# Performance work log

Hardware: AMD Instinct MI355X
Metric: run time of the kernel (lower is better)

Reference implementation:

```python
import jax, jax.numpy as jnp
import numpy as np

B, T, D, H = 128, 512, 1024, 1024


def setup_inputs() -> dict:
    key = jax.random.key(0)
    k_x, k_wx, k_wh = jax.random.split(key, 3)
    # PyTorch Linear init scale ~ U(-1/sqrt(fan_in), 1/sqrt(fan_in)); normal*0.03 is fine for a numeric baseline
    x = jax.random.normal(k_x, (B, T, D), dtype=jnp.float32)
    adjacency = jnp.zeros((T, T), dtype=jnp.float32)  # accepted by the torch module but unused
    Wx = jax.random.normal(k_wx, (4, D, H), dtype=jnp.float32) * (1.0 / np.sqrt(D))
    Wh = jax.random.normal(k_wh, (4, H, H), dtype=jnp.float32) * (1.0 / np.sqrt(H))
    b = jnp.zeros((4, H), dtype=jnp.float32)
    return {"x": x, "adjacency": adjacency, "Wx": Wx, "Wh": Wh, "b": b}


def _tree_lstm(x, Wx, Wh, b):
    # x: [B, T, D]; gate order: i, f, o, u
    xt = jnp.transpose(x, (1, 0, 2))  # [T, B, D]
    # precompute all input projections in one big batched GEMM: [T, 4, B, H]
    x_gates = jnp.einsum('tbd,gdh->tgbh', xt, Wx)
    h0 = jnp.zeros((x.shape[0], Wh.shape[1]), dtype=x.dtype)
    c0 = jnp.zeros_like(h0)

    def step(carry, xg_t):
        h, c = carry
        gates = xg_t + jnp.einsum('bh,ghk->gbk', h, Wh) + b[:, None, :]  # [4, B, H]
        i_t = jax.nn.sigmoid(gates[0])
        f_t = jax.nn.sigmoid(gates[1])
        o_t = jax.nn.sigmoid(gates[2])
        u_t = jnp.tanh(gates[3])
        c_new = f_t * c + i_t * u_t
        h_new = o_t * jnp.tanh(c_new)  # dropout is identity at inference
        return (h_new, c_new), None

    (h, _), _ = jax.lax.scan(step, (h0, c0), x_gates)
    return h  # [B, H]


def reference(x, adjacency, Wx, Wh, b):
    del adjacency  # unused in the original forward
    return _tree_lstm(x, Wx, Wh, b)
```

## Files before the change

kernel.cpp:

```cpp
#include <hip/hip_runtime.h>
#include <hip/hip_bf16.h>

typedef __attribute__((ext_vector_type(8))) short bf16x8;
typedef __attribute__((ext_vector_type(4))) float f32x4;
typedef __attribute__((ext_vector_type(2))) unsigned uint32x2;

#define NBLK 256
#define NTHR 512

__device__ __forceinline__ unsigned short f2bf(float f) {
  unsigned int u = __float_as_uint(f);
  unsigned int r = (u + 0x7FFFu + ((u >> 16) & 1u)) >> 16;
  return (unsigned short)r;
}

__device__ __forceinline__ bf16x8 ldg_b128_coh(const unsigned short* p) {
  bf16x8 r;
  asm volatile("global_load_dwordx4 %0, %1, off sc0 sc1"
               : "=v"(r) : "v"(p) : "memory");
  return r;
}
__device__ __forceinline__ void stg_b16_coh(unsigned short* p, unsigned v) {
  asm volatile("global_store_short %0, %1, off sc0 sc1"
               :: "v"(p), "v"(v) : "memory");
}

__global__ __launch_bounds__(256) void pack_w(const float* __restrict__ Wx,
                                              const float* __restrict__ Wh,
                                              unsigned short* __restrict__ Wp) {
  int idx = blockIdx.x * 256 + threadIdx.x;
  int k  = idx & 2047;
  int c  = (idx >> 11) & 31;
  int jb = idx >> 16;
  int g  = c & 3;
  int j  = jb * 8 + (c >> 2);
  float v = (k < 1024) ? Wh[((size_t)(g * 1024 + k)) * 1024 + j]
                       : Wx[((size_t)(g * 1024 + (k - 1024))) * 1024 + j];
  Wp[idx] = f2bf(v);
}

__global__ __launch_bounds__(256) void pack_x(const float* __restrict__ x,
                                              unsigned short* __restrict__ xpk) {
  size_t idx = (size_t)blockIdx.x * 256 + threadIdx.x;
  int lane = (int)(idx & 63);
  int wr   = (int)((idx >> 6) & 3);
  int s    = (int)((idx >> 8) & 15);
  int wn   = (int)((idx >> 12) & 1);
  int rb   = (int)((idx >> 13) & 1);
  int t    = (int)(idx >> 14);
  int a15 = lane & 15, hi = lane >> 4;
  int row = rb * 64 + wr * 16 + a15;
  int k   = (2 * s + wn) * 32 + hi * 8;
  const float* src = x + ((size_t)row * 512 + t) * 1024 + k;
  float4 f0 = *(const float4*)src;
  float4 f1 = *(const float4*)(src + 4);
  float fl[8] = {f0.x, f0.y, f0.z, f0.w, f1.x, f1.y, f1.z, f1.w};
  union { bf16x8 v; unsigned short us[8]; } u;
  #pragma unroll
  for (int e = 0; e < 8; ++e) u.us[e] = f2bf(fl[e]);
  *(bf16x8*)(xpk + idx * 8) = u.v;
}

__global__ __launch_bounds__(512, 2) void lstm_persist(
    const float* __restrict__ x,
    const unsigned short* __restrict__ xpk,
    const unsigned short* __restrict__ Wp,
    const float* __restrict__ bias,
    unsigned short* __restrict__ h0,
    unsigned short* __restrict__ h1,
    float* __restrict__ out,
    unsigned* __restrict__ bar)
{
  __shared__ unsigned short Wlds[32][2052];
  __shared__ float gt[2][64][33];

  const int tid = threadIdx.x;
  const int bx  = blockIdx.x;
  const int xcd = bx & 7;
  const int rb  = xcd >> 2;
  const int jb  = (bx >> 3) * 4 + (xcd & 3);
  const int row0 = rb * 64;

  #pragma unroll
  for (int rep = 0; rep < 16; ++rep) {
    int ch = rep * 512 + tid;
    int c  = ch >> 8;
    int k8 = (ch & 255) * 8;
    *(bf16x8*)&Wlds[c][k8] = *(const bf16x8*)(Wp + ((size_t)(jb * 32 + c)) * 2048 + k8);
  }

  const int lane = tid & 63;
  const int w    = tid >> 6;
  const int wr   = w >> 1;
  const int wn   = w & 1;
  const int a15  = lane & 15;
  const int hi   = lane >> 4;

  const int um  = tid >> 3;
  const int uj  = tid & 7;
  const int ujg = jb * 8 + uj;
  const float bi = bias[ujg], bf_ = bias[1024 + ujg];
  const float bo = bias[2048 + ujg], bu = bias[3072 + ujg];
  float creg = 0.f;

  const int rowg = row0 + wr * 16 + a15;
  const float* xrow = x + (size_t)rowg * 512 * 1024;
  const size_t xpk_lane = ((size_t)wr * 64 + lane) * 8;
  const unsigned* fpoll = bar + rb * 128 + (lane << 1);

  __syncthreads();

  unsigned short* hb[2] = {h0, h1};
  bf16x8 xreg[16];

  if (xpk) {
    const unsigned short* xs = xpk + (((size_t)0 * 2 + rb) * 2 + wn) * 16 * 2048 + xpk_lane;
    #pragma unroll
    for (int s = 0; s < 16; ++s)
      asm volatile("global_load_dwordx4 %0, %1, off" : "=v"(xreg[s]) : "v"(xs + s * 2048) : "memory");
    asm volatile("s_waitcnt vmcnt(0)" ::: "memory");
    __builtin_amdgcn_sched_barrier(0);
  } else {
    const float* xt = xrow + hi * 8;
    #pragma unroll
    for (int s = 0; s < 16; ++s) {
      const float* xp = xt + (2 * s + wn) * 32;
      float4 f0 = *(const float4*)xp;
      float4 f1 = *(const float4*)(xp + 4);
      float fl[8] = {f0.x, f0.y, f0.z, f0.w, f1.x, f1.y, f1.z, f1.w};
      union { bf16x8 v; unsigned short us[8]; } u;
      #pragma unroll
      for (int e = 0; e < 8; ++e) u.us[e] = f2bf(fl[e]);
      xreg[s] = u.v;
    }
  }

  for (int t = 0; t < 512; ++t) {
    const unsigned short* hc = hb[t & 1];
    unsigned short* hn = hb[(t + 1) & 1];

    bf16x8 hreg[16];
    const unsigned short* hbase = hc + (size_t)rowg * 1024 + hi * 8;
    #pragma unroll
    for (int s = 0; s < 16; ++s)
      hreg[s] = ldg_b128_coh(hbase + (2 * s + wn) * 32);
    __builtin_amdgcn_sched_barrier(0);

    f32x4 acc0 = {}, acc1 = {};
    #pragma unroll
    for (int s = 0; s < 16; ++s) {
      const int kk = 1024 + (2 * s + wn) * 32 + hi * 8;
      bf16x8 b0 = *(const bf16x8*)&Wlds[a15][kk];
      bf16x8 b1 = *(const bf16x8*)&Wlds[16 + a15][kk];
      acc0 = __builtin_amdgcn_mfma_f32_16x16x32_bf16(xreg[s], b0, acc0, 0, 0, 0);
      acc1 = __builtin_amdgcn_mfma_f32_16x16x32_bf16(xreg[s], b1, acc1, 0, 0, 0);
    }

    asm volatile("s_waitcnt vmcnt(8)" ::: "memory");
    __builtin_amdgcn_sched_barrier(0);
    #pragma unroll
    for (int s = 0; s < 8; ++s) {
      const int kk = (2 * s + wn) * 32 + hi * 8;
      bf16x8 b0 = *(const bf16x8*)&Wlds[a15][kk];
      bf16x8 b1 = *(const bf16x8*)&Wlds[16 + a15][kk];
      acc0 = __builtin_amdgcn_mfma_f32_16x16x32_bf16(hreg[s], b0, acc0, 0, 0, 0);
      acc1 = __builtin_amdgcn_mfma_f32_16x16x32_bf16(hreg[s], b1, acc1, 0, 0, 0);
    }
    asm volatile("s_waitcnt vmcnt(0)" ::: "memory");
    __builtin_amdgcn_sched_barrier(0);
    #pragma unroll
    for (int s = 8; s < 16; ++s) {
      const int kk = (2 * s + wn) * 32 + hi * 8;
      bf16x8 b0 = *(const bf16x8*)&Wlds[a15][kk];
      bf16x8 b1 = *(const bf16x8*)&Wlds[16 + a15][kk];
      acc0 = __builtin_amdgcn_mfma_f32_16x16x32_bf16(hreg[s], b0, acc0, 0, 0, 0);
      acc1 = __builtin_amdgcn_mfma_f32_16x16x32_bf16(hreg[s], b1, acc1, 0, 0, 0);
    }

    #pragma unroll
    for (int r = 0; r < 4; ++r) {
      gt[wn][wr * 16 + hi * 4 + r][a15]      = acc0[r];
      gt[wn][wr * 16 + hi * 4 + r][16 + a15] = acc1[r];
    }
    __syncthreads();

    float vi = gt[0][um][uj * 4 + 0] + gt[1][um][uj * 4 + 0] + bi;
    float vf = gt[0][um][uj * 4 + 1] + gt[1][um][uj * 4 + 1] + bf_;
    float vo = gt[0][um][uj * 4 + 2] + gt[1][um][uj * 4 + 2] + bo;
    float vu = gt[0][um][uj * 4 + 3] + gt[1][um][uj * 4 + 3] + bu;
    float iv = 1.f / (1.f + expf(-vi));
    float fv = 1.f / (1.f + expf(-vf));
    float ov = 1.f / (1.f + expf(-vo));
    float uv = tanhf(vu);
    creg = fv * creg + iv * uv;
    float hv = ov * tanhf(creg);
    stg_b16_coh(hn + (size_t)(row0 + um) * 1024 + ujg, (unsigned)f2bf(hv));
    if (t == 511) {
      out[(size_t)(row0 + um) * 1024 + ujg] = hv;
      break;
    }

    asm volatile("s_waitcnt vmcnt(0)" ::: "memory");
    __builtin_amdgcn_s_barrier();
    if (tid == 0) {
      const unsigned* p = bar + rb * 128 + jb;
      unsigned val = (unsigned)(t + 1);
      asm volatile("global_store_dword %0, %1, off sc0 sc1"
                   :: "v"(p), "v"(val) : "memory");
    }

    if (xpk) {
      const unsigned short* xs = xpk + (((size_t)(t + 1) * 2 + rb) * 2 + wn) * 16 * 2048 + xpk_lane;
      #pragma unroll
      for (int s = 0; s < 16; ++s)
        asm volatile("global_load_dwordx4 %0, %1, off" : "=v"(xreg[s]) : "v"(xs + s * 2048) : "memory");
    } else {
      const float* xt = xrow + (size_t)(t + 1) * 1024 + hi * 8;
      #pragma unroll
      for (int s = 0; s < 16; ++s) {
        const float* xp = xt + (2 * s + wn) * 32;
        float4 f0 = *(const float4*)xp;
        float4 f1 = *(const float4*)(xp + 4);
        float fl[8] = {f0.x, f0.y, f0.z, f0.w, f1.x, f1.y, f1.z, f1.w};
        union { bf16x8 v; unsigned short us[8]; } u;
        #pragma unroll
        for (int e = 0; e < 8; ++e) u.us[e] = f2bf(fl[e]);
        xreg[s] = u.v;
      }
    }

    for (;;) {
      uint32x2 v;
      asm volatile("global_load_dwordx2 %0, %1, off sc0 sc1"
                   : "=v"(v) : "v"(fpoll) : "memory");
      asm volatile("s_waitcnt vmcnt(0)" ::: "memory");
      if (__all(v.x > (unsigned)t && v.y > (unsigned)t)) break;
      __builtin_amdgcn_s_sleep(1);
    }
    __builtin_amdgcn_sched_barrier(0);
  }
}

extern "C" void kernel_launch(void* const* d_in, const int* in_sizes, int n_in,
                              void* d_out, int out_size, void* d_ws, size_t ws_size,
                              hipStream_t stream) {
  const float* x    = (const float*)d_in[0];
  const float* Wx   = (const float*)d_in[2];
  const float* Wh   = (const float*)d_in[3];
  const float* bias = (const float*)d_in[4];
  float* out = (float*)d_out;

  char* ws = (char*)d_ws;
  unsigned short* Wp = (unsigned short*)ws;
  unsigned short* h0 = (unsigned short*)(ws + 16777216);
  unsigned short* h1 = h0 + 128 * 1024;
  unsigned* bar = (unsigned*)(ws + 16777216 + 2 * 262144);
  const size_t XPK_OFF = 33554432;
  const size_t XPK_SZ  = 134217728;
  unsigned short* xpk = (ws_size >= XPK_OFF + XPK_SZ)
                        ? (unsigned short*)(ws + XPK_OFF) : nullptr;

  pack_w<<<32768, 256, 0, stream>>>(Wx, Wh, Wp);
  if (xpk) pack_x<<<32768, 256, 0, stream>>>(x, xpk);
  hipMemsetAsync(h0, 0, 128 * 1024 * sizeof(unsigned short), stream);
  hipMemsetAsync(bar, 0, 4096, stream);

  (void)in_sizes; (void)n_in;
  lstm_persist<<<NBLK, NTHR, 0, stream>>>(x, xpk, Wp, bias, h0, h1, out, bar);
}
```

Baseline: 3.797 ms.

## Use per-warp fine-grained flags and overlap x-projection with recurrent wait

Replaces the single per-block step flag with per-warp flags, so consumers poll flags for each K-chunk of h and issue loads for chunks as soon as their producers finish, instead of waiting for all blocks. The x-projection MFMAs for the next step are computed right after the gate update and prefetched two steps ahead, moving them off the critical path between barriers. Step 0 skips the h GEMM, so the h0 memset is dropped. This raises flag-polling traffic and control-flow complexity in exchange for less time waiting on the global barrier.

```diff
diff --git a/kernel.cpp b/kernel.cpp
--- a/kernel.cpp
+++ b/kernel.cpp
@@ -106,75 +106,101 @@
   const int rowg = row0 + wr * 16 + a15;
   const float* xrow = x + (size_t)rowg * 512 * 1024;
   const size_t xpk_lane = ((size_t)wr * 64 + lane) * 8;
-  const unsigned* fpoll = bar + rb * 128 + (lane << 1);
+
+  const unsigned* fp0 = bar + (rb * 8 + 2 * wr    ) * 128 + 2 * lane;
+  const unsigned* fp1 = bar + (rb * 8 + 2 * wr + 1) * 128 + 2 * lane;
+  unsigned* fprod = bar + (rb * 8 + w) * 128 + jb;
 
   __syncthreads();
 
   unsigned short* hb[2] = {h0, h1};
   bf16x8 xreg[16];
-
-  if (xpk) {
-    const unsigned short* xs = xpk + (((size_t)0 * 2 + rb) * 2 + wn) * 16 * 2048 + xpk_lane;
-    #pragma unroll
-    for (int s = 0; s < 16; ++s)
-      asm volatile("global_load_dwordx4 %0, %1, off" : "=v"(xreg[s]) : "v"(xs + s * 2048) : "memory");
-    asm volatile("s_waitcnt vmcnt(0)" ::: "memory");
-    __builtin_amdgcn_sched_barrier(0);
-  } else {
-    const float* xt = xrow + hi * 8;
-    #pragma unroll
-    for (int s = 0; s < 16; ++s) {
-      const float* xp = xt + (2 * s + wn) * 32;
-      float4 f0 = *(const float4*)xp;
-      float4 f1 = *(const float4*)(xp + 4);
-      float fl[8] = {f0.x, f0.y, f0.z, f0.w, f1.x, f1.y, f1.z, f1.w};
-      union { bf16x8 v; unsigned short us[8]; } u;
+  f32x4 acc0 = {}, acc1 = {};
+
+  auto xload = [&](int tt) {
+    if (xpk) {
+      const unsigned short* xs = xpk + ((((size_t)tt * 2 + rb) * 2 + wn) * 16) * 2048 + xpk_lane;
       #pragma unroll
-      for (int e = 0; e < 8; ++e) u.us[e] = f2bf(fl[e]);
-      xreg[s] = u.v;
-    }
+      for (int s = 0; s < 16; ++s)
+        asm volatile("global_load_dwordx4 %0, %1, off"
+                     : "=v"(xreg[s]) : "v"(xs + s * 2048) : "memory");
+    } else {
+      const float* xt = xrow + (size_t)tt * 1024 + hi * 8;
+      #pragma unroll
+      for (int s = 0; s < 16; ++s) {
+        const float* xp = xt + (2 * s + wn) * 32;
+        float4 f0 = *(const float4*)xp;
+        float4 f1 = *(const float4*)(xp + 4);
+        float fl[8] = {f0.x, f0.y, f0.z, f0.w, f1.x, f1.y, f1.z, f1.w};
+        union { bf16x8 v; unsigned short us[8]; } u;
+        #pragma unroll
+        for (int e = 0; e < 8; ++e) u.us[e] = f2bf(fl[e]);
+        xreg[s] = u.v;
+      }
+    }
+  };
+
+  xload(0);
+  asm volatile("s_waitcnt vmcnt(0)" ::: "memory");
+  __builtin_amdgcn_sched_barrier(0);
+  #pragma unroll
+  for (int s = 0; s < 16; ++s) {
+    const int kk = 1024 + (2 * s + wn) * 32 + hi * 8;
+    bf16x8 b0 = *(const bf16x8*)&Wlds[a15][kk];
+    bf16x8 b1 = *(const bf16x8*)&Wlds[16 + a15][kk];
+    acc0 = __builtin_amdgcn_mfma_f32_16x16x32_bf16(xreg[s], b0, acc0, 0, 0, 0);
+    acc1 = __builtin_amdgcn_mfma_f32_16x16x32_bf16(xreg[s], b1, acc1, 0, 0, 0);
   }
+  xload(1);
 
   for (int t = 0; t < 512; ++t) {
     const unsigned short* hc = hb[t & 1];
     unsigned short* hn = hb[(t + 1) & 1];
 
-    bf16x8 hreg[16];
-    const unsigned short* hbase = hc + (size_t)rowg * 1024 + hi * 8;
-    #pragma unroll
-    for (int s = 0; s < 16; ++s)
-      hreg[s] = ldg_b128_coh(hbase + (2 * s + wn) * 32);
-    __builtin_amdgcn_sched_barrier(0);
-
-    f32x4 acc0 = {}, acc1 = {};
-    #pragma unroll
-    for (int s = 0; s < 16; ++s) {
-      const int kk = 1024 + (2 * s + wn) * 32 + hi * 8;
-      bf16x8 b0 = *(const bf16x8*)&Wlds[a15][kk];
-      bf16x8 b1 = *(const bf16x8*)&Wlds[16 + a15][kk];
-      acc0 = __builtin_amdgcn_mfma_f32_16x16x32_bf16(xreg[s], b0, acc0, 0, 0, 0);
-      acc1 = __builtin_amdgcn_mfma_f32_16x16x32_bf16(xreg[s], b1, acc1, 0, 0, 0);
-    }
-
-    asm volatile("s_waitcnt vmcnt(8)" ::: "memory");
-    __builtin_amdgcn_sched_barrier(0);
-    #pragma unroll
-    for (int s = 0; s < 8; ++s) {
-      const int kk = (2 * s + wn) * 32 + hi * 8;
-      bf16x8 b0 = *(const bf16x8*)&Wlds[a15][kk];
-      bf16x8 b1 = *(const bf16x8*)&Wlds[16 + a15][kk];
-      acc0 = __builtin_amdgcn_mfma_f32_16x16x32_bf16(hreg[s], b0, acc0, 0, 0, 0);
-      acc1 = __builtin_amdgcn_mfma_f32_16x16x32_bf16(hreg[s], b1, acc1, 0, 0, 0);
-    }
-    asm volatile("s_waitcnt vmcnt(0)" ::: "memory");
-    __builtin_amdgcn_sched_barrier(0);
-    #pragma unroll
-    for (int s = 8; s < 16; ++s) {
-      const int kk = (2 * s + wn) * 32 + hi * 8;
-      bf16x8 b0 = *(const bf16x8*)&Wlds[a15][kk];
-      bf16x8 b1 = *(const bf16x8*)&Wlds[16 + a15][kk];
-      acc0 = __builtin_amdgcn_mfma_f32_16x16x32_bf16(hreg[s], b0, acc0, 0, 0, 0);
-      acc1 = __builtin_amdgcn_mfma_f32_16x16x32_bf16(hreg[s], b1, acc1, 0, 0, 0);
+    if (t > 0) {
+      bf16x8 hreg[16];
+      const unsigned short* hbase = hc + (size_t)rowg * 1024 + hi * 8;
+      unsigned remaining = 0xFFFFu;
+      while (remaining) {
+        uint32x2 v0, v1;
+        asm volatile("global_load_dwordx2 %0, %1, off sc0 sc1"
+                     : "=v"(v0) : "v"(fp0) : "memory");
+        asm volatile("global_load_dwordx2 %0, %1, off sc0 sc1"
+                     : "=v"(v1) : "v"(fp1) : "memory");
+        asm volatile("s_waitcnt vmcnt(0)" ::: "memory");
+        __builtin_amdgcn_sched_barrier(0);
+        int okA = (v0.x >= (unsigned)t) & (v1.x >= (unsigned)t);
+        int okB = (v0.y >= (unsigned)t) & (v1.y >= (unsigned)t);
+        unsigned long long be = __ballot(okA);
+        unsigned long long bo = __ballot(okB);
+        unsigned ready = 0;
+        #pragma unroll
+        for (int s = 0; s < 16; ++s) {
+          const int sh = (2 * s + wn) * 2;
+          unsigned g4 = ((unsigned)(be >> sh) & 3u) | ((((unsigned)(bo >> sh)) & 3u) << 2);
+          ready |= (g4 == 15u) ? (1u << s) : 0u;
+        }
+        unsigned newm = ready & remaining;
+        if (newm) {
+          #pragma unroll
+          for (int s = 0; s < 16; ++s)
+            if (newm & (1u << s))
+              hreg[s] = ldg_b128_coh(hbase + (2 * s + wn) * 32);
+          remaining &= ~newm;
+        } else {
+          __builtin_amdgcn_s_sleep(1);
+        }
+      }
+      asm volatile("s_waitcnt vmcnt(0)" ::: "memory");
+      __builtin_amdgcn_sched_barrier(0);
+      #pragma unroll
+      for (int s = 0; s < 16; ++s) {
+        const int kk = (2 * s + wn) * 32 + hi * 8;
+        bf16x8 b0 = *(const bf16x8*)&Wlds[a15][kk];
+        bf16x8 b1 = *(const bf16x8*)&Wlds[16 + a15][kk];
+        acc0 = __builtin_amdgcn_mfma_f32_16x16x32_bf16(hreg[s], b0, acc0, 0, 0, 0);
+        acc1 = __builtin_amdgcn_mfma_f32_16x16x32_bf16(hreg[s], b1, acc1, 0, 0, 0);
+      }
     }
 
     #pragma unroll
@@ -194,50 +220,33 @@
     float uv = tanhf(vu);
     creg = fv * creg + iv * uv;
     float hv = ov * tanhf(creg);
-    stg_b16_coh(hn + (size_t)(row0 + um) * 1024 + ujg, (unsigned)f2bf(hv));
     if (t == 511) {
       out[(size_t)(row0 + um) * 1024 + ujg] = hv;
-      break;
-    }
-
-    asm volatile("s_waitcnt vmcnt(0)" ::: "memory");
-    __builtin_amdgcn_s_barrier();
-    if (tid == 0) {
-      const unsigned* p = bar + rb * 128 + jb;
-      unsigned val = (unsigned)(t + 1);
-      asm volatile("global_store_dword %0, %1, off sc0 sc1"
-                   :: "v"(p), "v"(val) : "memory");
-    }
-
-    if (xpk) {
-      const unsigned short* xs = xpk + (((size_t)(t + 1) * 2 + rb) * 2 + wn) * 16 * 2048 + xpk_lane;
-      #pragma unroll
-      for (int s = 0; s < 16; ++s)
-        asm volatile("global_load_dwordx4 %0, %1, off" : "=v"(xreg[s]) : "v"(xs + s * 2048) : "memory");
     } else {
-      const float* xt = xrow + (size_t)(t + 1) * 1024 + hi * 8;
-      #pragma unroll
-      for (int s = 0; s < 16; ++s) {
-        const float* xp = xt + (2 * s + wn) * 32;
-        float4 f0 = *(const float4*)xp;
-        float4 f1 = *(const float4*)(xp + 4);
-        float fl[8] = {f0.x, f0.y, f0.z, f0.w, f1.x, f1.y, f1.z, f1.w};
-        union { bf16x8 v; unsigned short us[8]; } u;
-        #pragma unroll
-        for (int e = 0; e < 8; ++e) u.us[e] = f2bf(fl[e]);
-        xreg[s] = u.v;
-      }
-    }
-
-    for (;;) {
-      uint32x2 v;
-      asm volatile("global_load_dwordx2 %0, %1, off sc0 sc1"
-                   : "=v"(v) : "v"(fpoll) : "memory");
+      stg_b16_coh(hn + (size_t)(row0 + um) * 1024 + ujg, (unsigned)f2bf(hv));
       asm volatile("s_waitcnt vmcnt(0)" ::: "memory");
-      if (__all(v.x > (unsigned)t && v.y > (unsigned)t)) break;
-      __builtin_amdgcn_s_sleep(1);
-    }
+      if (lane == 0) {
+        unsigned val = (unsigned)(t + 1);
+        asm volatile("global_store_dword %0, %1, off sc0 sc1"
+                     :: "v"(fprod), "v"(val) : "memory");
+      }
+    }
+    __syncthreads();
+    if (t == 511) break;
+
     __builtin_amdgcn_sched_barrier(0);
+    f32x4 nacc0 = {}, nacc1 = {};
+    #pragma unroll
+    for (int s = 0; s < 16; ++s) {
+      const int kk = 1024 + (2 * s + wn) * 32 + hi * 8;
+      bf16x8 b0 = *(const bf16x8*)&Wlds[a15][kk];
+      bf16x8 b1 = *(const bf16x8*)&Wlds[16 + a15][kk];
+      nacc0 = __builtin_amdgcn_mfma_f32_16x16x32_bf16(xreg[s], b0, nacc0, 0, 0, 0);
+      nacc1 = __builtin_amdgcn_mfma_f32_16x16x32_bf16(xreg[s], b1, nacc1, 0, 0, 0);
+    }
+    acc0 = nacc0; acc1 = nacc1;
+
+    if (t + 2 < 512) xload(t + 2);
   }
 }
 
@@ -262,8 +271,7 @@
 
   pack_w<<<32768, 256, 0, stream>>>(Wx, Wh, Wp);
   if (xpk) pack_x<<<32768, 256, 0, stream>>>(x, xpk);
-  hipMemsetAsync(h0, 0, 128 * 1024 * sizeof(unsigned short), stream);
-  hipMemsetAsync(bar, 0, 4096, stream);
+  hipMemsetAsync(bar, 0, 8192, stream);
 
   (void)in_sizes; (void)n_in;
   lstm_persist<<<NBLK, NTHR, 0, stream>>>(x, xpk, Wp, bias, h0, h1, out, bar);
```

New measurement: 4.208 ms. 1.11x slower.
